# Kernel optimization log

Measured on AMD Instinct MI355X. Metric: run time of the kernel, lower is better.

The kernel has to match this reference:

```python
import jax, jax.numpy as jnp
import numpy as np

POS = np.array([[0,3,0.5],[0,3,1.5],[0,3,2.5],[0,3,3.5],[0,3,4.5],[0,3,5.5],[1,0,0],[1,6,6],[2,0,6],[2,6,0],[3,0,0],[3,6,6],[4,0,6],[4,6,0],[5,0,0],[5,6,6],[6,0,6],[6,6,0],[7,0,0],[7,6,6],[8,0,6],[8,6,0],[9,0,0],[9,6,6],[10,0,6],[10,6,0],[11,0,0],[11,6,6],[12,0,6],[12,6,0],[13,0,0],[13,6,6],[14,0,6],[14,6,0],[15,0,0],[15,6,6],[16,0,6],[16,6,0],[17,0.5,0.5],[17,3,0.5],[17,5.5,0.5],[17,0.5,3],[17,3,3],[17,5.5,3],[17,0.5,5.5],[17,3,5.5],[17,5.5,5.5]], dtype=np.float32)  # (47,3) fixed buffer

B, S, D, H, FF, HID = 512, 47, 32, 4, 2048, 256

def _ln(x, w, b, eps=1e-5):
    mu = jnp.mean(x, -1, keepdims=True)
    var = jnp.mean((x - mu) ** 2, -1, keepdims=True)
    return (x - mu) * jax.lax.rsqrt(var + eps) * w + b

def _encoder_layer(h, wi, bi, wo, bo, l1w, l1b, f1w, f1b, f2w, f2b, l2w, l2b):
    # torch post-norm TransformerEncoderLayer; batch_first=False => attention over axis 0
    L, N, E = h.shape
    Dh = E // H
    qkv = h @ wi.T + bi                                  # (L,N,3E)
    q, k, v = jnp.split(qkv, 3, axis=-1)
    q = q.reshape(L, N, H, Dh); k = k.reshape(L, N, H, Dh); v = v.reshape(L, N, H, Dh)
    scores = jnp.einsum('lnhd,mnhd->nhlm', q, k) * (1.0 / np.sqrt(Dh))  # (N,H,L,L)
    a = jax.nn.softmax(scores, axis=-1)
    o = jnp.einsum('nhlm,mnhd->lnhd', a, v).reshape(L, N, E)
    h = _ln(h + (o @ wo.T + bo), l1w, l1b)
    ff = jax.nn.relu(h @ f1w.T + f1b) @ f2w.T + f2b
    return _ln(h + ff, l2w, l2b)

def setup_inputs():
    key = jax.random.key(0)
    ks = list(jax.random.split(key, 24))
    rn = lambda k, s, sc=0.05: jax.random.normal(k, s, jnp.float32) * sc
    return dict(
        x=jax.random.normal(ks[0], (B, S), jnp.float32),
        w_in=rn(ks[1], (D, 1)), b_in=rn(ks[2], (D,)),
        w_pos=rn(ks[3], (D, 3)), b_pos=rn(ks[4], (D,)),
        cls_token=rn(ks[5], (1, 1, D), 1.0),
        attn_in_w=rn(ks[6], (2, 3 * D, D)), attn_in_b=rn(ks[7], (2, 3 * D)),
        attn_out_w=rn(ks[8], (2, D, D)), attn_out_b=rn(ks[9], (2, D)),
        ln1_w=jnp.ones((2, D)), ln1_b=jnp.zeros((2, D)),
        ff1_w=rn(ks[10], (2, FF, D)), ff1_b=rn(ks[11], (2, FF)),
        ff2_w=rn(ks[12], (2, D, FF)), ff2_b=rn(ks[13], (2, D)),
        ln2_w=jnp.ones((2, D)), ln2_b=jnp.zeros((2, D)),
        out_w=rn(ks[14], (1, D)), out_b=rn(ks[15], (1,)),
        mlp_w0=rn(ks[16], (HID, S)), mlp_b0=rn(ks[17], (HID,)),
        mlp_w1=rn(ks[18], (HID, HID)), mlp_b1=rn(ks[19], (HID,)),
        mlp_w2=rn(ks[20], (1, HID)), mlp_b2=rn(ks[21], (1,)),
    )

def reference(x, w_in, b_in, w_pos, b_pos, cls_token, attn_in_w, attn_in_b, attn_out_w, attn_out_b, ln1_w, ln1_b, ff1_w, ff1_b, ff2_w, ff2_b, ln2_w, ln2_b, out_w, out_b, mlp_w0, mlp_b0, mlp_w1, mlp_b1, mlp_w2, mlp_b2):
    Bn = x.shape[0]
    h = x[..., None] * w_in[:, 0] + b_in                 # Linear(1,D): (B,S,D)
    h = h + (jnp.asarray(POS) @ w_pos.T + b_pos)         # pos projection (S,D)
    cls = jnp.broadcast_to(cls_token, (Bn, 1, D))
    h = jnp.concatenate([cls, h], axis=1)                # (B,S+1,D)
    for i in range(2):
        h = _encoder_layer(h, attn_in_w[i], attn_in_b[i], attn_out_w[i], attn_out_b[i], ln1_w[i], ln1_b[i], ff1_w[i], ff1_b[i], ff2_w[i], ff2_b[i], ln2_w[i], ln2_b[i])
    out = jax.nn.relu(h[:, 1:, :] @ out_w.T + out_b)[..., 0]   # (B,S); dropout = eval identity
    o = jax.nn.relu(out @ mlp_w0.T + mlp_b0)
    o = jax.nn.relu(o @ mlp_w1.T + mlp_b1)
    o = jax.nn.relu(o @ mlp_w2.T + mlp_b2)               # MLP ends with ReLU per source
    return o
```

## Files before the change

### kernel.cpp

```cpp
#include <hip/hip_runtime.h>

#define NB 512
#define NS 47
#define NP 48
#define DIM 32
#define NFF 2048
#define NHID 256
#define NROWS (NB * NP)
#define FTOK 48

#define VSTR 520
#define PSTR 72

typedef _Float16 f16x8 __attribute__((ext_vector_type(8)));
typedef _Float16 f16x4 __attribute__((ext_vector_type(4)));
typedef float f32x4 __attribute__((ext_vector_type(4)));

__constant__ float POSC[NS * 3] = {
  0,3,0.5f, 0,3,1.5f, 0,3,2.5f, 0,3,3.5f, 0,3,4.5f, 0,3,5.5f,
  1,0,0, 1,6,6, 2,0,6, 2,6,0, 3,0,0, 3,6,6, 4,0,6, 4,6,0,
  5,0,0, 5,6,6, 6,0,6, 6,6,0, 7,0,0, 7,6,6, 8,0,6, 8,6,0,
  9,0,0, 9,6,6, 10,0,6, 10,6,0, 11,0,0, 11,6,6, 12,0,6, 12,6,0,
  13,0,0, 13,6,6, 14,0,6, 14,6,0, 15,0,0, 15,6,6, 16,0,6, 16,6,0,
  17,0.5f,0.5f, 17,3,0.5f, 17,5.5f,0.5f, 17,0.5f,3, 17,3,3, 17,5.5f,3,
  17,0.5f,5.5f, 17,3,5.5f, 17,5.5f,5.5f
};

__global__ __launch_bounds__(256) void prep_embed_kernel(
    const float* __restrict__ w1, const float* __restrict__ w2,
    _Float16* __restrict__ w1h, _Float16* __restrict__ w2h,
    const float* __restrict__ x, const float* __restrict__ w_in,
    const float* __restrict__ b_in, const float* __restrict__ w_pos,
    const float* __restrict__ b_pos, const float* __restrict__ cls,
    float* __restrict__ h) {
  const int bx = blockIdx.x;
  if (bx < 512) {
    int idx = bx * 256 + threadIdx.x;
    w1h[idx] = (_Float16)w1[idx];
    int l = idx >> 16, r = idx & 65535, d = r >> 11, ff = r & 2047;
    int dst = ((l * 64 + (ff >> 5)) * 32 + d) * 32 + (ff & 31);
    w2h[dst] = (_Float16)w2[idx];
    return;
  }
  int idx = (bx - 512) * 256 + threadIdx.x;
  int r = idx >> 5, d = idx & 31;
  int l = r / NP, n = r - l * NP;
  float v;
  if (n == 0) {
    v = cls[d];
  } else {
    int s = n - 1;
    v = x[l * NS + s] * w_in[d] + b_in[d]
      + POSC[s * 3 + 0] * w_pos[d * 3 + 0]
      + POSC[s * 3 + 1] * w_pos[d * 3 + 1]
      + POSC[s * 3 + 2] * w_pos[d * 3 + 2] + b_pos[d];
  }
  h[idx] = v;
}

__global__ __launch_bounds__(256) void kv_kernel(
    const float* __restrict__ h, const float* __restrict__ wi, const float* __restrict__ bi,
    _Float16* __restrict__ Kp, _Float16* __restrict__ Vt) {
  __shared__ float ws_[512];
  __shared__ float bs_[16];
  const int t = threadIdx.x;
  const int nh = blockIdx.x >> 1;
  const int n = nh >> 2, hh = nh & 3;
  const int l = ((blockIdx.x & 1) << 8) | t;
  for (int i = t; i < 512; i += 256) {
    int sub = i >> 8, rem = i & 255;
    int jj = rem >> 5, d = rem & 31;
    ws_[i] = wi[((sub + 1) * 32 + hh * 8 + jj) * 32 + d];
  }
  if (t < 16) bs_[t] = bi[((t >> 3) + 1) * 32 + hh * 8 + (t & 7)];
  __syncthreads();
  const float4* hrow = (const float4*)(h + (l * NP + n) * 32);
  float4 hv[8];
  #pragma unroll
  for (int i = 0; i < 8; ++i) hv[i] = hrow[i];
  f16x8 kh, kl_, vh;
  #pragma unroll
  for (int jj = 0; jj < 8; ++jj) {
    float k0 = bs_[jj], k1 = 0.f, k2 = 0.f, k3 = 0.f;
    float v0 = bs_[8 + jj], v1 = 0.f, v2 = 0.f, v3 = 0.f;
    #pragma unroll
    for (int d4 = 0; d4 < 8; ++d4) {
      float4 hvv = hv[d4];
      k0 += hvv.x * ws_[jj * 32 + 4 * d4 + 0];
      k1 += hvv.y * ws_[jj * 32 + 4 * d4 + 1];
      k2 += hvv.z * ws_[jj * 32 + 4 * d4 + 2];
      k3 += hvv.w * ws_[jj * 32 + 4 * d4 + 3];
      v0 += hvv.x * ws_[256 + jj * 32 + 4 * d4 + 0];
      v1 += hvv.y * ws_[256 + jj * 32 + 4 * d4 + 1];
      v2 += hvv.z * ws_[256 + jj * 32 + 4 * d4 + 2];
      v3 += hvv.w * ws_[256 + jj * 32 + 4 * d4 + 3];
    }
    float kv = (k0 + k1) + (k2 + k3);
    float vv = (v0 + v1) + (v2 + v3);
    kh[jj] = (_Float16)kv; kl_[jj] = (_Float16)(kv - (float)kh[jj]);
    vh[jj] = (_Float16)vv;
  }
  _Float16* kdst = Kp + ((size_t)nh * 512 + l) * 16;
  *(f16x8*)(kdst) = kh;
  *(f16x8*)(kdst + 8) = kl_;
  #pragma unroll
  for (int d = 0; d < 8; ++d) Vt[(size_t)nh * 4096 + d * 512 + l] = vh[d];
}

__global__ __launch_bounds__(256, 3) void attn_mfma_kernel(
    const float* __restrict__ h, const float* __restrict__ wi, const float* __restrict__ bi,
    const _Float16* __restrict__ Kp, const _Float16* __restrict__ Vt,
    float* __restrict__ o) {
  __shared__ alignas(16) _Float16 khi[512 * 8];
  __shared__ alignas(16) _Float16 klo[512 * 8];
  __shared__ alignas(16) _Float16 vts[8 * VSTR];
  __shared__ alignas(16) float hq_pls[4608];
  __shared__ alignas(16) _Float16 qf[128 * 16];
  __shared__ float wsq[256];
  __shared__ float bq[8];
  const int bx = blockIdx.x;
  const int nh = bx >> 2, qc = bx & 3;
  const int n = nh >> 2, hh = nh & 3;
  const int t = threadIdx.x;
  const int lane = t & 63, wv = t >> 6;
  const int c = lane & 15, g = lane >> 4;

  const _Float16* kg = Kp + (size_t)nh * 8192;
  for (int r = t; r < 512; r += 256) {
    const uint4* src = (const uint4*)(kg + r * 16);
    uint4 a = src[0], b = src[1];
    *(uint4*)(khi + r * 8) = a;
    *(uint4*)(klo + r * 8) = b;
  }
  {
    const _Float16* vg = Vt + (size_t)nh * 4096;
    for (int i = t; i < 512; i += 256) {
      int d = i >> 6, seg = i & 63;
      *(uint4*)(vts + d * VSTR + seg * 8) = *(const uint4*)(vg + d * 512 + seg * 8);
    }
  }
  wsq[t] = wi[(hh * 8 + (t & 7)) * 32 + (t >> 3)];
  if (t < 8) bq[t] = bi[hh * 8 + t];
  float* hq = hq_pls;

  #pragma unroll
  for (int rp = 0; rp < 2; ++rp) {
    {
      int row = t >> 2, quar = t & 3;
      const float4* src =
          (const float4*)(h + (((qc * 128 + rp * 64 + row) * NP) + n) * 32 + quar * 8);
      float4 a = src[0], b = src[1];
      __syncthreads();
      *(float4*)(hq + row * 36 + quar * 8) = a;
      *(float4*)(hq + row * 36 + quar * 8 + 4) = b;
    }
    __syncthreads();
    {
      int row = t >> 2, pr = t & 3;
      #pragma unroll
      for (int u = 0; u < 2; ++u) {
        int jj = pr * 2 + u;
        float a = bq[jj];
        #pragma unroll
        for (int d = 0; d < 32; ++d) a += hq[row * 36 + d] * wsq[d * 8 + jj];
        _Float16 qh = (_Float16)a;
        _Float16 ql = (_Float16)(a - (float)qh);
        qf[(rp * 64 + row) * 16 + jj] = qh;
        qf[(rp * 64 + row) * 16 + 8 + jj] = ql;
      }
    }
    __syncthreads();
  }

  const f16x8 hz = {(_Float16)0,(_Float16)0,(_Float16)0,(_Float16)0,
                    (_Float16)0,(_Float16)0,(_Float16)0,(_Float16)0};
  const f32x4 zf = {0.f, 0.f, 0.f, 0.f};
  _Float16* pls_ = (_Float16*)hq_pls;
  _Float16* mypA = pls_ + wv * (16 * PSTR);
  _Float16* mypB = pls_ + (4 + wv) * (16 * PSTR);
  const int q0A = qc * 128 + wv * 16;
  const int q0B = q0A + 64;

  f16x8 aqA = hz, aqB = hz;
  if (g < 3) {
    aqA = *(const f16x8*)(qf + (wv * 16 + c) * 16 + (g & 1) * 8);
    aqB = *(const f16x8*)(qf + (64 + wv * 16 + c) * 16 + (g & 1) * 8);
  }
  f32x4 accA = {0.f, 0.f, 0.f, 0.f}, accB = {0.f, 0.f, 0.f, 0.f};
  float lsA[4] = {0.f, 0.f, 0.f, 0.f}, lsB[4] = {0.f, 0.f, 0.f, 0.f};

  for (int ch = 0; ch < 8; ++ch) {
    const int kb = ch * 64;
    #pragma unroll
    for (int kt = 0; kt < 4; ++kt) {
      f16x8 bk = hz;
      if (g < 2)       bk = *(const f16x8*)(khi + (kb + kt * 16 + c) * 8);
      else if (g == 2) bk = *(const f16x8*)(klo + (kb + kt * 16 + c) * 8);
      f32x4 sA = __builtin_amdgcn_mfma_f32_16x16x32_f16(aqA, bk, zf, 0, 0, 0);
      f32x4 sB = __builtin_amdgcn_mfma_f32_16x16x32_f16(aqB, bk, zf, 0, 0, 0);
      #pragma unroll
      for (int r = 0; r < 4; ++r) {
        float pA = __expf(sA[r] * 0.35355339059327373f - 2.0f);
        float pB = __expf(sB[r] * 0.35355339059327373f - 2.0f);
        _Float16 phA = (_Float16)pA;
        _Float16 phB = (_Float16)pB;
        lsA[r] += (float)phA;
        lsB[r] += (float)phB;
        mypA[(g * 4 + r) * PSTR + kt * 16 + c] = phA;
        mypB[(g * 4 + r) * PSTR + kt * 16 + c] = phB;
      }
    }
    #pragma unroll
    for (int half = 0; half < 2; ++half) {
      f16x8 bv = hz;
      if (c < 8) bv = *(const f16x8*)(vts + c * VSTR + kb + half * 32 + g * 8);
      f16x8 apA = *(const f16x8*)(mypA + c * PSTR + half * 32 + g * 8);
      f16x8 apB = *(const f16x8*)(mypB + c * PSTR + half * 32 + g * 8);
      accA = __builtin_amdgcn_mfma_f32_16x16x32_f16(apA, bv, accA, 0, 0, 0);
      accB = __builtin_amdgcn_mfma_f32_16x16x32_f16(apB, bv, accB, 0, 0, 0);
    }
  }
  #pragma unroll
  for (int m = 1; m < 16; m <<= 1) {
    #pragma unroll
    for (int r = 0; r < 4; ++r) {
      lsA[r] += __shfl_xor(lsA[r], m, 64);
      lsB[r] += __shfl_xor(lsB[r], m, 64);
    }
  }
  if (c < 8) {
    #pragma unroll
    for (int r = 0; r < 4; ++r) {
      o[((q0A + g * 4 + r) * NP + n) * 32 + hh * 8 + c] = accA[r] / lsA[r];
      o[((q0B + g * 4 + r) * NP + n) * 32 + hh * 8 + c] = accB[r] / lsB[r];
    }
  }
}

__global__ __launch_bounds__(256) void proj_ln1_kernel(
    const float* __restrict__ o, const float* __restrict__ wo, const float* __restrict__ bo,
    const float* __restrict__ lw, const float* __restrict__ lb, float* __restrict__ h) {
  __shared__ float wos[32 * 33];
  __shared__ float pre[64 * 33];
  const int g = blockIdx.x, t = threadIdx.x;
  for (int i = t; i < 1024; i += 256) wos[(i >> 5) * 33 + (i & 31)] = wo[i];
  __syncthreads();
  const int subr = t >> 2, jq = t & 3;
  const int r = g * 64 + subr;
  const float4* orow = (const float4*)(o + r * 32);
  float4 ov[8];
  #pragma unroll
  for (int i = 0; i < 8; ++i) ov[i] = orow[i];
  const float* hres = h + r * 32 + jq * 8;
  #pragma unroll
  for (int jj = 0; jj < 8; ++jj) {
    int j = jq * 8 + jj;
    float a0 = bo[j], a1 = 0.f, a2 = 0.f, a3 = 0.f;
    #pragma unroll
    for (int d4 = 0; d4 < 8; ++d4) {
      float4 vv = ov[d4];
      a0 += vv.x * wos[j * 33 + 4 * d4 + 0];
      a1 += vv.y * wos[j * 33 + 4 * d4 + 1];
      a2 += vv.z * wos[j * 33 + 4 * d4 + 2];
      a3 += vv.w * wos[j * 33 + 4 * d4 + 3];
    }
    pre[subr * 33 + j] = (a0 + a1) + (a2 + a3) + hres[jj];
  }
  __syncthreads();
  if (t < 64) {
    float mu = 0.f;
    #pragma unroll
    for (int d = 0; d < 32; ++d) mu += pre[t * 33 + d];
    mu *= (1.f / 32.f);
    float var = 0.f;
    #pragma unroll
    for (int d = 0; d < 32; ++d) { float dv = pre[t * 33 + d] - mu; var += dv * dv; }
    float rs = rsqrtf(var * (1.f / 32.f) + 1e-5f);
    float* hrow = h + (g * 64 + t) * 32;
    #pragma unroll
    for (int d = 0; d < 32; ++d)
      hrow[d] = (pre[t * 33 + d] - mu) * rs * lw[d] + lb[d];
  }
}

__global__ __launch_bounds__(256, 2) void ff_fused_kernel(
    const float* __restrict__ h, const _Float16* __restrict__ w1h,
    const float* __restrict__ b1, const _Float16* __restrict__ w2h,
    const float* __restrict__ b2, const float* __restrict__ lw,
    const float* __restrict__ lb, const float* __restrict__ ow,
    const float* __restrict__ ob,
    const float* __restrict__ m0w, const float* __restrict__ m0b,
    const float* __restrict__ m1w, const float* __restrict__ m1b,
    const float* __restrict__ m2w, const float* __restrict__ m2b,
    float* __restrict__ out, int do_head) {
  __shared__ alignas(16) float yw[4][FTOK * 33];
  __shared__ alignas(16) float pre_s[FTOK * 33];
  __shared__ float sv1[48];
  __shared__ float hid[NHID];
  __shared__ float red[4];
  const int t = threadIdx.x;
  const int lane = t & 63;
  const int wv = t >> 6;
  const int nl = lane & 15;
  const int g = lane >> 4;
  const int g4 = g * 4;
  const int r0 = blockIdx.x * FTOK;

  f16x8 hfrag[3];
  #pragma unroll
  for (int tt = 0; tt < 3; ++tt) {
    const float4 h0 = *(const float4*)(h + (r0 + tt * 16 + nl) * 32 + g * 8);
    const float4 h1 = *(const float4*)(h + (r0 + tt * 16 + nl) * 32 + g * 8 + 4);
    hfrag[tt][0] = (_Float16)h0.x; hfrag[tt][1] = (_Float16)h0.y;
    hfrag[tt][2] = (_Float16)h0.z; hfrag[tt][3] = (_Float16)h0.w;
    hfrag[tt][4] = (_Float16)h1.x; hfrag[tt][5] = (_Float16)h1.y;
    hfrag[tt][6] = (_Float16)h1.z; hfrag[tt][7] = (_Float16)h1.w;
  }

  f32x4 acc0[3], acc1[3];
  #pragma unroll
  for (int tt = 0; tt < 3; ++tt) {
    acc0[tt] = (f32x4){0.f, 0.f, 0.f, 0.f};
    acc1[tt] = (f32x4){0.f, 0.f, 0.f, 0.f};
  }
  const f32x4 zero = {0.f, 0.f, 0.f, 0.f};

  for (int sc = 0; sc < 16; ++sc) {
    const int ffb = wv * 512 + sc * 32;
    f16x8 wf0 = *(const f16x8*)(w1h + (ffb + nl) * 32 + g * 8);
    f16x8 wf1 = *(const f16x8*)(w1h + (ffb + 16 + nl) * 32 + g * 8);
    float4 bv0 = *(const float4*)(b1 + ffb + g4);
    float4 bv1 = *(const float4*)(b1 + ffb + 16 + g4);
    const _Float16* cb = w2h + (ffb >> 5) * 1024;
    f16x4 a0lo = *(const f16x4*)(cb + nl * 32 + g4);
    f16x4 a0hi = *(const f16x4*)(cb + nl * 32 + 16 + g4);
    f16x4 a1lo = *(const f16x4*)(cb + (16 + nl) * 32 + g4);
    f16x4 a1hi = *(const f16x4*)(cb + (16 + nl) * 32 + 16 + g4);
    f16x8 A0, A1;
    #pragma unroll
    for (int j = 0; j < 4; ++j) {
      A0[j] = a0lo[j]; A0[4 + j] = a0hi[j];
      A1[j] = a1lo[j]; A1[4 + j] = a1hi[j];
    }
    #pragma unroll
    for (int tt = 0; tt < 3; ++tt) {
      f32x4 cc0 = __builtin_amdgcn_mfma_f32_16x16x32_f16(wf0, hfrag[tt], zero, 0, 0, 0);
      f32x4 cc1 = __builtin_amdgcn_mfma_f32_16x16x32_f16(wf1, hfrag[tt], zero, 0, 0, 0);
      f16x8 uB;
      uB[0] = (_Float16)fmaxf(cc0[0] + bv0.x, 0.f);
      uB[1] = (_Float16)fmaxf(cc0[1] + bv0.y, 0.f);
      uB[2] = (_Float16)fmaxf(cc0[2] + bv0.z, 0.f);
      uB[3] = (_Float16)fmaxf(cc0[3] + bv0.w, 0.f);
      uB[4] = (_Float16)fmaxf(cc1[0] + bv1.x, 0.f);
      uB[5] = (_Float16)fmaxf(cc1[1] + bv1.y, 0.f);
      uB[6] = (_Float16)fmaxf(cc1[2] + bv1.z, 0.f);
      uB[7] = (_Float16)fmaxf(cc1[3] + bv1.w, 0.f);
      acc0[tt] = __builtin_amdgcn_mfma_f32_16x16x32_f16(A0, uB, acc0[tt], 0, 0, 0);
      acc1[tt] = __builtin_amdgcn_mfma_f32_16x16x32_f16(A1, uB, acc1[tt], 0, 0, 0);
    }
  }
  #pragma unroll
  for (int tt = 0; tt < 3; ++tt) {
    #pragma unroll
    for (int r = 0; r < 4; ++r) {
      yw[wv][(tt * 16 + nl) * 33 + g4 + r]      = acc0[tt][r];
      yw[wv][(tt * 16 + nl) * 33 + 16 + g4 + r] = acc1[tt][r];
    }
  }
  __syncthreads();

  {
    int idx = t;
    #pragma unroll
    for (int u = 0; u < 6; ++u, idx += 256) {
      int tok = idx >> 5, d = idx & 31;
      int off = tok * 33 + d;
      float v = yw[0][off] + yw[1][off] + yw[2][off] + yw[3][off]
              + b2[d] + h[(r0 + tok) * 32 + d];
      pre_s[off] = v;
    }
  }
  __syncthreads();

  if (t < FTOK) {
    float mu = 0.f;
    #pragma unroll
    for (int d = 0; d < 32; ++d) mu += pre_s[t * 33 + d];
    mu *= (1.f / 32.f);
    float var = 0.f;
    #pragma unroll
    for (int d = 0; d < 32; ++d) { float dv = pre_s[t * 33 + d] - mu; var += dv * dv; }
    float rs = rsqrtf(var * (1.f / 32.f) + 1e-5f);
    const int rr = r0 + t;
    float* hrow = (float*)h + (size_t)rr * 32;
    float hn[32];
    #pragma unroll
    for (int d = 0; d < 32; ++d) {
      hn[d] = (pre_s[t * 33 + d] - mu) * rs * lw[d] + lb[d];
      hrow[d] = hn[d];
    }
    if (do_head && t > 0) {
      float a = ob[0];
      #pragma unroll
      for (int d = 0; d < 32; ++d) a += hn[d] * ow[d];
      sv1[t - 1] = fmaxf(a, 0.f);
    }
  }

  if (do_head) {
    __syncthreads();
    const int l = blockIdx.x;
    {
      float a = m0b[t];
      const float* wr = m0w + t * NS;
      #pragma unroll
      for (int s = 0; s < NS; ++s) a += sv1[s] * wr[s];
      hid[t] = fmaxf(a, 0.f);
    }
    __syncthreads();
    {
      float a = m1b[t];
      const float4* wr = (const float4*)(m1w + t * NHID);
      #pragma unroll 8
      for (int j4 = 0; j4 < 64; ++j4) {
        float4 w = wr[j4];
        a += hid[4 * j4 + 0] * w.x + hid[4 * j4 + 1] * w.y
           + hid[4 * j4 + 2] * w.z + hid[4 * j4 + 3] * w.w;
      }
      float h2 = fmaxf(a, 0.f);
      float part = h2 * m2w[t];
      #pragma unroll
      for (int off = 32; off > 0; off >>= 1) part += __shfl_down(part, off, 64);
      if ((t & 63) == 0) red[t >> 6] = part;
    }
    __syncthreads();
    if (t == 0) out[l] = fmaxf(red[0] + red[1] + red[2] + red[3] + m2b[0], 0.f);
  }
}

extern "C" void kernel_launch(void* const* d_in, const int* in_sizes, int n_in,
                              void* d_out, int out_size, void* d_ws, size_t ws_size,
                              hipStream_t stream) {
  (void)in_sizes; (void)n_in; (void)out_size; (void)ws_size;
  const float* x     = (const float*)d_in[0];
  const float* w_in  = (const float*)d_in[1];
  const float* b_in  = (const float*)d_in[2];
  const float* w_pos = (const float*)d_in[3];
  const float* b_pos = (const float*)d_in[4];
  const float* cls   = (const float*)d_in[5];
  const float* wi    = (const float*)d_in[6];
  const float* bi    = (const float*)d_in[7];
  const float* wo    = (const float*)d_in[8];
  const float* bo    = (const float*)d_in[9];
  const float* l1w   = (const float*)d_in[10];
  const float* l1b   = (const float*)d_in[11];
  const float* f1w   = (const float*)d_in[12];
  const float* f1b   = (const float*)d_in[13];
  const float* f2w   = (const float*)d_in[14];
  const float* f2b   = (const float*)d_in[15];
  const float* l2w   = (const float*)d_in[16];
  const float* l2b   = (const float*)d_in[17];
  const float* ow    = (const float*)d_in[18];
  const float* ob    = (const float*)d_in[19];
  const float* m0w   = (const float*)d_in[20];
  const float* m0b   = (const float*)d_in[21];
  const float* m1w   = (const float*)d_in[22];
  const float* m1b   = (const float*)d_in[23];
  const float* m2w   = (const float*)d_in[24];
  const float* m2b   = (const float*)d_in[25];
  float* out = (float*)d_out;

  float* ws   = (float*)d_ws;
  float* h    = ws;
  float* o    = ws + 786432;
  float* R2   = ws + 1572864;
  _Float16* Kp = (_Float16*)R2;
  _Float16* Vt = (_Float16*)(R2 + 786432);
  _Float16* w1h = (_Float16*)(ws + 2776576);
  _Float16* w2h = (_Float16*)(ws + 2842112);

  prep_embed_kernel<<<3584, 256, 0, stream>>>(f1w, f2w, w1h, w2h,
                                              x, w_in, b_in, w_pos, b_pos, cls, h);
  for (int L = 0; L < 2; ++L) {
    kv_kernel<<<384, 256, 0, stream>>>(h, wi + L * 3072, bi + L * 96, Kp, Vt);
    attn_mfma_kernel<<<768, 256, 0, stream>>>(h, wi + L * 3072, bi + L * 96, Kp, Vt, o);
    proj_ln1_kernel<<<384, 256, 0, stream>>>(o, wo + L * 1024, bo + L * 32,
                                             l1w + L * 32, l1b + L * 32, h);
    ff_fused_kernel<<<512, 256, 0, stream>>>(h, w1h + L * 65536, f1b + L * NFF,
                                             w2h + L * 65536, f2b + L * 32,
                                             l2w + L * 32, l2b + L * 32,
                                             ow, ob, m0w, m0b, m1w, m1b, m2w, m2b,
                                             out, L);
  }
}
```

Before: 150.6 us.

## Double-buffer FF weight chunks into LDS with async global_load_lds prefetch

The fused feed-forward kernel now stages each wave's W1 and W2 fp16 weight chunks in a double-buffered shared-memory area. It uses asynchronous global-to-LDS loads, prefetching chunk sc+1 while chunk sc runs through the MFMA loop. The goal is to hide global and L2 latency on the weight reads that previously went straight into registers each iteration. In exchange it adds 32KB of LDS per block, which may limit occupancy, and a block-wide barrier every iteration even though each wave only uses its own slice.

New measurement: 151.7 us. No clear change (+0.7%).

```diff
diff --git a/kernel.cpp b/kernel.cpp
--- a/kernel.cpp
+++ b/kernel.cpp
@@ -15,6 +15,11 @@
 typedef _Float16 f16x8 __attribute__((ext_vector_type(8)));
 typedef _Float16 f16x4 __attribute__((ext_vector_type(4)));
 typedef float f32x4 __attribute__((ext_vector_type(4)));
+
+#define GLL(gsrc, ldst)                                                     \
+  __builtin_amdgcn_global_load_lds(                                         \
+      (const __attribute__((address_space(1))) void*)(gsrc),                \
+      (__attribute__((address_space(3))) void*)(ldst), 16, 0, 0)
 
 __constant__ float POSC[NS * 3] = {
   0,3,0.5f, 0,3,1.5f, 0,3,2.5f, 0,3,3.5f, 0,3,4.5f, 0,3,5.5f,
@@ -293,6 +298,7 @@
     const float* __restrict__ m1w, const float* __restrict__ m1b,
     const float* __restrict__ m2w, const float* __restrict__ m2b,
     float* __restrict__ out, int do_head) {
+  __shared__ alignas(16) _Float16 wbuf[2 * 4 * 2048];
   __shared__ alignas(16) float yw[4][FTOK * 33];
   __shared__ alignas(16) float pre_s[FTOK * 33];
   __shared__ float sv1[48];
@@ -317,6 +323,17 @@
     hfrag[tt][6] = (_Float16)h1.z; hfrag[tt][7] = (_Float16)h1.w;
   }
 
+  {
+    const _Float16* g1 = w1h + (wv * 512) * 32;
+    const _Float16* g2 = w2h + (wv * 16) * 1024;
+    _Float16* d = wbuf + wv * 2048;
+    GLL(g1 + lane * 8,       d);
+    GLL(g1 + 512 + lane * 8, d + 512);
+    GLL(g2 + lane * 8,       d + 1024);
+    GLL(g2 + 512 + lane * 8, d + 1536);
+  }
+  __syncthreads();
+
   f32x4 acc0[3], acc1[3];
   #pragma unroll
   for (int tt = 0; tt < 3; ++tt) {
@@ -326,12 +343,19 @@
   const f32x4 zero = {0.f, 0.f, 0.f, 0.f};
 
   for (int sc = 0; sc < 16; ++sc) {
-    const int ffb = wv * 512 + sc * 32;
-    f16x8 wf0 = *(const f16x8*)(w1h + (ffb + nl) * 32 + g * 8);
-    f16x8 wf1 = *(const f16x8*)(w1h + (ffb + 16 + nl) * 32 + g * 8);
-    float4 bv0 = *(const float4*)(b1 + ffb + g4);
-    float4 bv1 = *(const float4*)(b1 + ffb + 16 + g4);
-    const _Float16* cb = w2h + (ffb >> 5) * 1024;
+    if (sc < 15) {
+      const _Float16* g1 = w1h + (wv * 512 + (sc + 1) * 32) * 32;
+      const _Float16* g2 = w2h + (wv * 16 + (sc + 1)) * 1024;
+      _Float16* d = wbuf + ((sc + 1) & 1) * 8192 + wv * 2048;
+      GLL(g1 + lane * 8,       d);
+      GLL(g1 + 512 + lane * 8, d + 512);
+      GLL(g2 + lane * 8,       d + 1024);
+      GLL(g2 + 512 + lane * 8, d + 1536);
+    }
+    const _Float16* s1 = wbuf + (sc & 1) * 8192 + wv * 2048;
+    f16x8 wf0 = *(const f16x8*)(s1 + nl * 32 + g * 8);
+    f16x8 wf1 = *(const f16x8*)(s1 + 512 + nl * 32 + g * 8);
+    const _Float16* cb = s1 + 1024;
     f16x4 a0lo = *(const f16x4*)(cb + nl * 32 + g4);
     f16x4 a0hi = *(const f16x4*)(cb + nl * 32 + 16 + g4);
     f16x4 a1lo = *(const f16x4*)(cb + (16 + nl) * 32 + g4);
@@ -342,6 +366,9 @@
       A0[j] = a0lo[j]; A0[4 + j] = a0hi[j];
       A1[j] = a1lo[j]; A1[4 + j] = a1hi[j];
     }
+    const int ffb = wv * 512 + sc * 32;
+    float4 bv0 = *(const float4*)(b1 + ffb + g4);
+    float4 bv1 = *(const float4*)(b1 + ffb + 16 + g4);
     #pragma unroll
     for (int tt = 0; tt < 3; ++tt) {
       f32x4 cc0 = __builtin_amdgcn_mfma_f32_16x16x32_f16(wf0, hfrag[tt], zero, 0, 0, 0);
@@ -358,7 +385,9 @@
       acc0[tt] = __builtin_amdgcn_mfma_f32_16x16x32_f16(A0, uB, acc0[tt], 0, 0, 0);
       acc1[tt] = __builtin_amdgcn_mfma_f32_16x16x32_f16(A1, uB, acc1[tt], 0, 0, 0);
     }
-  }
+    __syncthreads();
+  }
+
   #pragma unroll
   for (int tt = 0; tt < 3; ++tt) {
     #pragma unroll
```

## Merge all stages into one cooperative persistent megakernel with grid syncs

Applied to the files above, without the earlier changes.

Turns the prep, kv, attention, projection+LN and FFN kernels into device functions and runs them from a single cooperative kernel. Stages are separated by grid-wide barriers and blocks loop over virtual block indices, with a shared-memory arena reused across stages. The aim is to remove per-launch overhead and inter-kernel gaps across nine launches. In exchange, every stage is capped at the occupancy of the largest-LDS stage (at most 512 blocks), and it pays grid.sync costs. The old multi-kernel path remains as a fallback if the cooperative launch fails.

Measured after the change: 477.0 us. 217% more time.

```diff
diff --git a/kernel.cpp b/kernel.cpp
--- a/kernel.cpp
+++ b/kernel.cpp
@@ -1,4 +1,7 @@
 #include <hip/hip_runtime.h>
+#include <hip/hip_cooperative_groups.h>
+
+namespace cg = cooperative_groups;
 
 #define NB 512
 #define NS 47
@@ -6,7 +9,6 @@
 #define DIM 32
 #define NFF 2048
 #define NHID 256
-#define NROWS (NB * NP)
 #define FTOK 48
 
 #define VSTR 520
@@ -26,47 +28,47 @@
   17,0.5f,5.5f, 17,3,5.5f, 17,5.5f,5.5f
 };
 
-__global__ __launch_bounds__(256) void prep_embed_kernel(
-    const float* __restrict__ w1, const float* __restrict__ w2,
-    _Float16* __restrict__ w1h, _Float16* __restrict__ w2h,
-    const float* __restrict__ x, const float* __restrict__ w_in,
-    const float* __restrict__ b_in, const float* __restrict__ w_pos,
-    const float* __restrict__ b_pos, const float* __restrict__ cls,
-    float* __restrict__ h) {
-  const int bx = blockIdx.x;
-  if (bx < 512) {
-    int idx = bx * 256 + threadIdx.x;
-    w1h[idx] = (_Float16)w1[idx];
+struct MKArgs {
+  const float *x, *w_in, *b_in, *w_pos, *b_pos, *cls;
+  const float *wi, *bi, *wo, *bo, *l1w, *l1b, *f1w, *f1b, *f2w, *f2b, *l2w, *l2b;
+  const float *ow, *ob, *m0w, *m0b, *m1w, *m1b, *m2w, *m2b;
+  float *h, *o, *out;
+  _Float16 *Kp, *Vt, *w1h, *w2h;
+};
+
+
+__device__ __forceinline__ void prep_embed_body(const MKArgs& a, int vb, int t) {
+  if (vb < 512) {
+    int idx = vb * 256 + t;
+    a.w1h[idx] = (_Float16)a.f1w[idx];
     int l = idx >> 16, r = idx & 65535, d = r >> 11, ff = r & 2047;
     int dst = ((l * 64 + (ff >> 5)) * 32 + d) * 32 + (ff & 31);
-    w2h[dst] = (_Float16)w2[idx];
+    a.w2h[dst] = (_Float16)a.f2w[idx];
     return;
   }
-  int idx = (bx - 512) * 256 + threadIdx.x;
+  int idx = (vb - 512) * 256 + t;
   int r = idx >> 5, d = idx & 31;
   int l = r / NP, n = r - l * NP;
   float v;
   if (n == 0) {
-    v = cls[d];
+    v = a.cls[d];
   } else {
     int s = n - 1;
-    v = x[l * NS + s] * w_in[d] + b_in[d]
-      + POSC[s * 3 + 0] * w_pos[d * 3 + 0]
-      + POSC[s * 3 + 1] * w_pos[d * 3 + 1]
-      + POSC[s * 3 + 2] * w_pos[d * 3 + 2] + b_pos[d];
-  }
-  h[idx] = v;
-}
-
-__global__ __launch_bounds__(256) void kv_kernel(
-    const float* __restrict__ h, const float* __restrict__ wi, const float* __restrict__ bi,
-    _Float16* __restrict__ Kp, _Float16* __restrict__ Vt) {
-  __shared__ float ws_[512];
-  __shared__ float bs_[16];
-  const int t = threadIdx.x;
-  const int nh = blockIdx.x >> 1;
+    v = a.x[l * NS + s] * a.w_in[d] + a.b_in[d]
+      + POSC[s * 3 + 0] * a.w_pos[d * 3 + 0]
+      + POSC[s * 3 + 1] * a.w_pos[d * 3 + 1]
+      + POSC[s * 3 + 2] * a.w_pos[d * 3 + 2] + a.b_pos[d];
+  }
+  a.h[idx] = v;
+}
+
+__device__ __forceinline__ void kv_body(const MKArgs& a, const float* wi,
+                                        const float* bi, int vb, int t, char* arena) {
+  float* ws_ = (float*)arena;
+  float* bs_ = (float*)(arena + 2048);
+  const int nh = vb >> 1;
   const int n = nh >> 2, hh = nh & 3;
-  const int l = ((blockIdx.x & 1) << 8) | t;
+  const int l = ((vb & 1) << 8) | t;
   for (int i = t; i < 512; i += 256) {
     int sub = i >> 8, rem = i & 255;
     int jj = rem >> 5, d = rem & 31;
@@ -74,7 +76,7 @@
   }
   if (t < 16) bs_[t] = bi[((t >> 3) + 1) * 32 + hh * 8 + (t & 7)];
   __syncthreads();
-  const float4* hrow = (const float4*)(h + (l * NP + n) * 32);
+  const float4* hrow = (const float4*)(a.h + (l * NP + n) * 32);
   float4 hv[8];
   #pragma unroll
   for (int i = 0; i < 8; ++i) hv[i] = hrow[i];
@@ -100,40 +102,36 @@
     kh[jj] = (_Float16)kv; kl_[jj] = (_Float16)(kv - (float)kh[jj]);
     vh[jj] = (_Float16)vv;
   }
-  _Float16* kdst = Kp + ((size_t)nh * 512 + l) * 16;
+  _Float16* kdst = a.Kp + ((size_t)nh * 512 + l) * 16;
   *(f16x8*)(kdst) = kh;
   *(f16x8*)(kdst + 8) = kl_;
   #pragma unroll
-  for (int d = 0; d < 8; ++d) Vt[(size_t)nh * 4096 + d * 512 + l] = vh[d];
-}
-
-__global__ __launch_bounds__(256, 3) void attn_mfma_kernel(
-    const float* __restrict__ h, const float* __restrict__ wi, const float* __restrict__ bi,
-    const _Float16* __restrict__ Kp, const _Float16* __restrict__ Vt,
-    float* __restrict__ o) {
-  __shared__ alignas(16) _Float16 khi[512 * 8];
-  __shared__ alignas(16) _Float16 klo[512 * 8];
-  __shared__ alignas(16) _Float16 vts[8 * VSTR];
-  __shared__ alignas(16) float hq_pls[4608];
-  __shared__ alignas(16) _Float16 qf[128 * 16];
-  __shared__ float wsq[256];
-  __shared__ float bq[8];
-  const int bx = blockIdx.x;
-  const int nh = bx >> 2, qc = bx & 3;
+  for (int d = 0; d < 8; ++d) a.Vt[(size_t)nh * 4096 + d * 512 + l] = vh[d];
+}
+
+__device__ __forceinline__ void attn_body(const MKArgs& a, const float* wi,
+                                          const float* bi, int vb, int t, char* arena) {
+  _Float16* khi = (_Float16*)arena;
+  _Float16* klo = (_Float16*)(arena + 8192);
+  _Float16* vts = (_Float16*)(arena + 16384);
+  float* hq_pls = (float*)(arena + 24704);
+  _Float16* qf  = (_Float16*)(arena + 43136);
+  float* wsq    = (float*)(arena + 47232);
+  float* bq     = (float*)(arena + 48256);
+  const int nh = vb >> 2, qc = vb & 3;
   const int n = nh >> 2, hh = nh & 3;
-  const int t = threadIdx.x;
   const int lane = t & 63, wv = t >> 6;
   const int c = lane & 15, g = lane >> 4;
 
-  const _Float16* kg = Kp + (size_t)nh * 8192;
+  const _Float16* kg = a.Kp + (size_t)nh * 8192;
   for (int r = t; r < 512; r += 256) {
     const uint4* src = (const uint4*)(kg + r * 16);
-    uint4 a = src[0], b = src[1];
-    *(uint4*)(khi + r * 8) = a;
-    *(uint4*)(klo + r * 8) = b;
+    uint4 aa = src[0], bb = src[1];
+    *(uint4*)(khi + r * 8) = aa;
+    *(uint4*)(klo + r * 8) = bb;
   }
   {
-    const _Float16* vg = Vt + (size_t)nh * 4096;
+    const _Float16* vg = a.Vt + (size_t)nh * 4096;
     for (int i = t; i < 512; i += 256) {
       int d = i >> 6, seg = i & 63;
       *(uint4*)(vts + d * VSTR + seg * 8) = *(const uint4*)(vg + d * 512 + seg * 8);
@@ -148,11 +146,11 @@
     {
       int row = t >> 2, quar = t & 3;
       const float4* src =
-          (const float4*)(h + (((qc * 128 + rp * 64 + row) * NP) + n) * 32 + quar * 8);
-      float4 a = src[0], b = src[1];
+          (const float4*)(a.h + (((qc * 128 + rp * 64 + row) * NP) + n) * 32 + quar * 8);
+      float4 aa = src[0], bb = src[1];
       __syncthreads();
-      *(float4*)(hq + row * 36 + quar * 8) = a;
-      *(float4*)(hq + row * 36 + quar * 8 + 4) = b;
+      *(float4*)(hq + row * 36 + quar * 8) = aa;
+      *(float4*)(hq + row * 36 + quar * 8 + 4) = bb;
     }
     __syncthreads();
     {
@@ -160,11 +158,11 @@
       #pragma unroll
       for (int u = 0; u < 2; ++u) {
         int jj = pr * 2 + u;
-        float a = bq[jj];
+        float av = bq[jj];
         #pragma unroll
-        for (int d = 0; d < 32; ++d) a += hq[row * 36 + d] * wsq[d * 8 + jj];
-        _Float16 qh = (_Float16)a;
-        _Float16 ql = (_Float16)(a - (float)qh);
+        for (int d = 0; d < 32; ++d) av += hq[row * 36 + d] * wsq[d * 8 + jj];
+        _Float16 qh = (_Float16)av;
+        _Float16 ql = (_Float16)(av - (float)qh);
         qf[(rp * 64 + row) * 16 + jj] = qh;
         qf[(rp * 64 + row) * 16 + 8 + jj] = ql;
       }
@@ -231,27 +229,26 @@
   if (c < 8) {
     #pragma unroll
     for (int r = 0; r < 4; ++r) {
-      o[((q0A + g * 4 + r) * NP + n) * 32 + hh * 8 + c] = accA[r] / lsA[r];
-      o[((q0B + g * 4 + r) * NP + n) * 32 + hh * 8 + c] = accB[r] / lsB[r];
-    }
-  }
-}
-
-__global__ __launch_bounds__(256) void proj_ln1_kernel(
-    const float* __restrict__ o, const float* __restrict__ wo, const float* __restrict__ bo,
-    const float* __restrict__ lw, const float* __restrict__ lb, float* __restrict__ h) {
-  __shared__ float wos[32 * 33];
-  __shared__ float pre[64 * 33];
-  const int g = blockIdx.x, t = threadIdx.x;
+      a.o[((q0A + g * 4 + r) * NP + n) * 32 + hh * 8 + c] = accA[r] / lsA[r];
+      a.o[((q0B + g * 4 + r) * NP + n) * 32 + hh * 8 + c] = accB[r] / lsB[r];
+    }
+  }
+}
+
+__device__ __forceinline__ void proj_body(const MKArgs& a, const float* wo,
+                                          const float* bo, const float* lw,
+                                          const float* lb, int vb, int t, char* arena) {
+  float* wos = (float*)arena;
+  float* pre = (float*)(arena + 4224);
   for (int i = t; i < 1024; i += 256) wos[(i >> 5) * 33 + (i & 31)] = wo[i];
   __syncthreads();
   const int subr = t >> 2, jq = t & 3;
-  const int r = g * 64 + subr;
-  const float4* orow = (const float4*)(o + r * 32);
+  const int r = vb * 64 + subr;
+  const float4* orow = (const float4*)(a.o + r * 32);
   float4 ov[8];
   #pragma unroll
   for (int i = 0; i < 8; ++i) ov[i] = orow[i];
-  const float* hres = h + r * 32 + jq * 8;
+  const float* hres = a.h + r * 32 + jq * 8;
   #pragma unroll
   for (int jj = 0; jj < 8; ++jj) {
     int j = jq * 8 + jj;
@@ -276,41 +273,35 @@
     #pragma unroll
     for (int d = 0; d < 32; ++d) { float dv = pre[t * 33 + d] - mu; var += dv * dv; }
     float rs = rsqrtf(var * (1.f / 32.f) + 1e-5f);
-    float* hrow = h + (g * 64 + t) * 32;
+    float* hrow = a.h + (vb * 64 + t) * 32;
     #pragma unroll
     for (int d = 0; d < 32; ++d)
       hrow[d] = (pre[t * 33 + d] - mu) * rs * lw[d] + lb[d];
   }
 }
 
-__global__ __launch_bounds__(256, 2) void ff_fused_kernel(
-    const float* __restrict__ h, const _Float16* __restrict__ w1h,
-    const float* __restrict__ b1, const _Float16* __restrict__ w2h,
-    const float* __restrict__ b2, const float* __restrict__ lw,
-    const float* __restrict__ lb, const float* __restrict__ ow,
-    const float* __restrict__ ob,
-    const float* __restrict__ m0w, const float* __restrict__ m0b,
-    const float* __restrict__ m1w, const float* __restrict__ m1b,
-    const float* __restrict__ m2w, const float* __restrict__ m2b,
-    float* __restrict__ out, int do_head) {
-  __shared__ alignas(16) float yw[4][FTOK * 33];
-  __shared__ alignas(16) float pre_s[FTOK * 33];
-  __shared__ float sv1[48];
-  __shared__ float hid[NHID];
-  __shared__ float red[4];
-  const int t = threadIdx.x;
+__device__ __forceinline__ void ff_body(const MKArgs& a, const _Float16* w1h,
+                                        const float* b1, const _Float16* w2h,
+                                        const float* b2, const float* lw,
+                                        const float* lb, int do_head, int vb,
+                                        int t, char* arena) {
+  float* yw    = (float*)arena;
+  float* pre_s = (float*)(arena + 25344);
+  float* sv1   = (float*)(arena + 31680);
+  float* hid   = (float*)(arena + 31872);
+  float* red   = (float*)(arena + 32896);
   const int lane = t & 63;
   const int wv = t >> 6;
   const int nl = lane & 15;
   const int g = lane >> 4;
   const int g4 = g * 4;
-  const int r0 = blockIdx.x * FTOK;
+  const int r0 = vb * FTOK;
 
   f16x8 hfrag[3];
   #pragma unroll
   for (int tt = 0; tt < 3; ++tt) {
-    const float4 h0 = *(const float4*)(h + (r0 + tt * 16 + nl) * 32 + g * 8);
-    const float4 h1 = *(const float4*)(h + (r0 + tt * 16 + nl) * 32 + g * 8 + 4);
+    const float4 h0 = *(const float4*)(a.h + (r0 + tt * 16 + nl) * 32 + g * 8);
+    const float4 h1 = *(const float4*)(a.h + (r0 + tt * 16 + nl) * 32 + g * 8 + 4);
     hfrag[tt][0] = (_Float16)h0.x; hfrag[tt][1] = (_Float16)h0.y;
     hfrag[tt][2] = (_Float16)h0.z; hfrag[tt][3] = (_Float16)h0.w;
     hfrag[tt][4] = (_Float16)h1.x; hfrag[tt][5] = (_Float16)h1.y;
@@ -363,8 +354,8 @@
   for (int tt = 0; tt < 3; ++tt) {
     #pragma unroll
     for (int r = 0; r < 4; ++r) {
-      yw[wv][(tt * 16 + nl) * 33 + g4 + r]      = acc0[tt][r];
-      yw[wv][(tt * 16 + nl) * 33 + 16 + g4 + r] = acc1[tt][r];
+      yw[wv * (FTOK * 33) + (tt * 16 + nl) * 33 + g4 + r]      = acc0[tt][r];
+      yw[wv * (FTOK * 33) + (tt * 16 + nl) * 33 + 16 + g4 + r] = acc1[tt][r];
     }
   }
   __syncthreads();
@@ -375,8 +366,8 @@
     for (int u = 0; u < 6; ++u, idx += 256) {
       int tok = idx >> 5, d = idx & 31;
       int off = tok * 33 + d;
-      float v = yw[0][off] + yw[1][off] + yw[2][off] + yw[3][off]
-              + b2[d] + h[(r0 + tok) * 32 + d];
+      float v = yw[off] + yw[FTOK * 33 + off] + yw[2 * FTOK * 33 + off]
+              + yw[3 * FTOK * 33 + off] + b2[d] + a.h[(r0 + tok) * 32 + d];
       pre_s[off] = v;
     }
   }
@@ -392,7 +383,7 @@
     for (int d = 0; d < 32; ++d) { float dv = pre_s[t * 33 + d] - mu; var += dv * dv; }
     float rs = rsqrtf(var * (1.f / 32.f) + 1e-5f);
     const int rr = r0 + t;
-    float* hrow = (float*)h + (size_t)rr * 32;
+    float* hrow = a.h + (size_t)rr * 32;
     float hn[32];
     #pragma unroll
     for (int d = 0; d < 32; ++d) {
@@ -400,96 +391,163 @@
       hrow[d] = hn[d];
     }
     if (do_head && t > 0) {
-      float a = ob[0];
+      float av = a.ob[0];
       #pragma unroll
-      for (int d = 0; d < 32; ++d) a += hn[d] * ow[d];
-      sv1[t - 1] = fmaxf(a, 0.f);
+      for (int d = 0; d < 32; ++d) av += hn[d] * a.ow[d];
+      sv1[t - 1] = fmaxf(av, 0.f);
     }
   }
 
   if (do_head) {
     __syncthreads();
-    const int l = blockIdx.x;
+    const int l = vb;
     {
-      float a = m0b[t];
-      const float* wr = m0w + t * NS;
+      float av = a.m0b[t];
+      const float* wr = a.m0w + t * NS;
       #pragma unroll
-      for (int s = 0; s < NS; ++s) a += sv1[s] * wr[s];
-      hid[t] = fmaxf(a, 0.f);
+      for (int s = 0; s < NS; ++s) av += sv1[s] * wr[s];
+      hid[t] = fmaxf(av, 0.f);
     }
     __syncthreads();
     {
-      float a = m1b[t];
-      const float4* wr = (const float4*)(m1w + t * NHID);
+      float av = a.m1b[t];
+      const float4* wr = (const float4*)(a.m1w + t * NHID);
       #pragma unroll 8
       for (int j4 = 0; j4 < 64; ++j4) {
         float4 w = wr[j4];
-        a += hid[4 * j4 + 0] * w.x + hid[4 * j4 + 1] * w.y
-           + hid[4 * j4 + 2] * w.z + hid[4 * j4 + 3] * w.w;
+        av += hid[4 * j4 + 0] * w.x + hid[4 * j4 + 1] * w.y
+            + hid[4 * j4 + 2] * w.z + hid[4 * j4 + 3] * w.w;
       }
-      float h2 = fmaxf(a, 0.f);
-      float part = h2 * m2w[t];
+      float h2 = fmaxf(av, 0.f);
+      float part = h2 * a.m2w[t];
       #pragma unroll
       for (int off = 32; off > 0; off >>= 1) part += __shfl_down(part, off, 64);
       if ((t & 63) == 0) red[t >> 6] = part;
     }
     __syncthreads();
-    if (t == 0) out[l] = fmaxf(red[0] + red[1] + red[2] + red[3] + m2b[0], 0.f);
-  }
+    if (t == 0) a.out[l] = fmaxf(red[0] + red[1] + red[2] + red[3] + a.m2b[0], 0.f);
+  }
+}
+
+__global__ __launch_bounds__(256, 2) void megakernel(MKArgs a) {
+  __shared__ alignas(16) char arena[48384];
+  cg::grid_group grid = cg::this_grid();
+  const int bid = blockIdx.x;
+  const int nblk = gridDim.x;
+  const int t = threadIdx.x;
+
+  for (int vb = bid; vb < 3584; vb += nblk) prep_embed_body(a, vb, t);
+  grid.sync();
+
+  for (int L = 0; L < 2; ++L) {
+    const float* wiL = a.wi + L * 3072;
+    const float* biL = a.bi + L * 96;
+    for (int vb = bid; vb < 384; vb += nblk) {
+      kv_body(a, wiL, biL, vb, t, arena);
+      __syncthreads();
+    }
+    grid.sync();
+    for (int vb = bid; vb < 768; vb += nblk) {
+      attn_body(a, wiL, biL, vb, t, arena);
+      __syncthreads();
+    }
+    grid.sync();
+    for (int vb = bid; vb < 384; vb += nblk) {
+      proj_body(a, a.wo + L * 1024, a.bo + L * 32,
+                a.l1w + L * 32, a.l1b + L * 32, vb, t, arena);
+      __syncthreads();
+    }
+    grid.sync();
+    for (int vb = bid; vb < 512; vb += nblk) {
+      ff_body(a, a.w1h + L * 65536, a.f1b + L * NFF, a.w2h + L * 65536,
+              a.f2b + L * 32, a.l2w + L * 32, a.l2b + L * 32, L, vb, t, arena);
+      __syncthreads();
+    }
+    if (L == 0) grid.sync();
+  }
+}
+
+__global__ __launch_bounds__(256) void prep_embed_kernel(MKArgs a) {
+  prep_embed_body(a, blockIdx.x, threadIdx.x);
+}
+__global__ __launch_bounds__(256) void kv_kernel(MKArgs a, int L) {
+  __shared__ alignas(16) char arena[2112];
+  kv_body(a, a.wi + L * 3072, a.bi + L * 96, blockIdx.x, threadIdx.x, arena);
+}
+__global__ __launch_bounds__(256, 3) void attn_kernel(MKArgs a, int L) {
+  __shared__ alignas(16) char arena[48288];
+  attn_body(a, a.wi + L * 3072, a.bi + L * 96, blockIdx.x, threadIdx.x, arena);
+}
+__global__ __launch_bounds__(256) void proj_kernel(MKArgs a, int L) {
+  __shared__ alignas(16) char arena[12672];
+  proj_body(a, a.wo + L * 1024, a.bo + L * 32, a.l1w + L * 32, a.l1b + L * 32,
+            blockIdx.x, threadIdx.x, arena);
+}
+__global__ __launch_bounds__(256, 2) void ff_kernel(MKArgs a, int L) {
+  __shared__ alignas(16) char arena[32912];
+  ff_body(a, a.w1h + L * 65536, a.f1b + L * NFF, a.w2h + L * 65536,
+          a.f2b + L * 32, a.l2w + L * 32, a.l2b + L * 32, L,
+          blockIdx.x, threadIdx.x, arena);
 }
 
 extern "C" void kernel_launch(void* const* d_in, const int* in_sizes, int n_in,
                               void* d_out, int out_size, void* d_ws, size_t ws_size,
                               hipStream_t stream) {
   (void)in_sizes; (void)n_in; (void)out_size; (void)ws_size;
-  const float* x     = (const float*)d_in[0];
-  const float* w_in  = (const float*)d_in[1];
-  const float* b_in  = (const float*)d_in[2];
-  const float* w_pos = (const float*)d_in[3];
-  const float* b_pos = (const float*)d_in[4];
-  const float* cls   = (const float*)d_in[5];
-  const float* wi    = (const float*)d_in[6];
-  const float* bi    = (const float*)d_in[7];
-  const float* wo    = (const float*)d_in[8];
-  const float* bo    = (const float*)d_in[9];
-  const float* l1w   = (const float*)d_in[10];
-  const float* l1b   = (const float*)d_in[11];
-  const float* f1w   = (const float*)d_in[12];
-  const float* f1b   = (const float*)d_in[13];
-  const float* f2w   = (const float*)d_in[14];
-  const float* f2b   = (const float*)d_in[15];
-  const float* l2w   = (const float*)d_in[16];
-  const float* l2b   = (const float*)d_in[17];
-  const float* ow    = (const float*)d_in[18];
-  const float* ob    = (const float*)d_in[19];
-  const float* m0w   = (const float*)d_in[20];
-  const float* m0b   = (const float*)d_in[21];
-  const float* m1w   = (const float*)d_in[22];
-  const float* m1b   = (const float*)d_in[23];
-  const float* m2w   = (const float*)d_in[24];
-  const float* m2b   = (const float*)d_in[25];
-  float* out = (float*)d_out;
-
-  float* ws   = (float*)d_ws;
-  float* h    = ws;
-  float* o    = ws + 786432;
-  float* R2   = ws + 1572864;
-  _Float16* Kp = (_Float16*)R2;
-  _Float16* Vt = (_Float16*)(R2 + 786432);
-  _Float16* w1h = (_Float16*)(ws + 2776576);
-  _Float16* w2h = (_Float16*)(ws + 2842112);
-
-  prep_embed_kernel<<<3584, 256, 0, stream>>>(f1w, f2w, w1h, w2h,
-                                              x, w_in, b_in, w_pos, b_pos, cls, h);
-  for (int L = 0; L < 2; ++L) {
-    kv_kernel<<<384, 256, 0, stream>>>(h, wi + L * 3072, bi + L * 96, Kp, Vt);
-    attn_mfma_kernel<<<768, 256, 0, stream>>>(h, wi + L * 3072, bi + L * 96, Kp, Vt, o);
-    proj_ln1_kernel<<<384, 256, 0, stream>>>(o, wo + L * 1024, bo + L * 32,
-                                             l1w + L * 32, l1b + L * 32, h);
-    ff_fused_kernel<<<512, 256, 0, stream>>>(h, w1h + L * 65536, f1b + L * NFF,
-                                             w2h + L * 65536, f2b + L * 32,
-                                             l2w + L * 32, l2b + L * 32,
-                                             ow, ob, m0w, m0b, m1w, m1b, m2w, m2b,
-                                             out, L);
-  }
-}
+  float* ws = (float*)d_ws;
+  MKArgs a;
+  a.x     = (const float*)d_in[0];
+  a.w_in  = (const float*)d_in[1];
+  a.b_in  = (const float*)d_in[2];
+  a.w_pos = (const float*)d_in[3];
+  a.b_pos = (const float*)d_in[4];
+  a.cls   = (const float*)d_in[5];
+  a.wi    = (const float*)d_in[6];
+  a.bi    = (const float*)d_in[7];
+  a.wo    = (const float*)d_in[8];
+  a.bo    = (const float*)d_in[9];
+  a.l1w   = (const float*)d_in[10];
+  a.l1b   = (const float*)d_in[11];
+  a.f1w   = (const float*)d_in[12];
+  a.f1b   = (const float*)d_in[13];
+  a.f2w   = (const float*)d_in[14];
+  a.f2b   = (const float*)d_in[15];
+  a.l2w   = (const float*)d_in[16];
+  a.l2b   = (const float*)d_in[17];
+  a.ow    = (const float*)d_in[18];
+  a.ob    = (const float*)d_in[19];
+  a.m0w   = (const float*)d_in[20];
+  a.m0b   = (const float*)d_in[21];
+  a.m1w   = (const float*)d_in[22];
+  a.m1b   = (const float*)d_in[23];
+  a.m2w   = (const float*)d_in[24];
+  a.m2b   = (const float*)d_in[25];
+  a.out   = (float*)d_out;
+  a.h     = ws;
+  a.o     = ws + 786432;
+  a.Kp    = (_Float16*)(ws + 1572864);
+  a.Vt    = (_Float16*)(ws + 1572864 + 786432);
+  a.w1h   = (_Float16*)(ws + 2776576);
+  a.w2h   = (_Float16*)(ws + 2842112);
+
+  int occ = 0;
+  hipError_t err = hipErrorUnknown;
+  hipError_t eo = hipOccupancyMaxActiveBlocksPerMultiprocessor(
+      &occ, (const void*)megakernel, 256, 0);
+  if (eo == hipSuccess && occ > 0) {
+    int nblk = occ * 256;
+    if (nblk > 512) nblk = 512;
+    void* kp[] = {(void*)&a};
+    err = hipLaunchCooperativeKernel((const void*)megakernel, dim3(nblk),
+                                     dim3(256), kp, 0, stream);
+  }
+  if (err != hipSuccess) {
+    prep_embed_kernel<<<3584, 256, 0, stream>>>(a);
+    for (int L = 0; L < 2; ++L) {
+      kv_kernel<<<384, 256, 0, stream>>>(a, L);
+      attn_kernel<<<768, 256, 0, stream>>>(a, L);
+      proj_kernel<<<384, 256, 0, stream>>>(a, L);
+      ff_kernel<<<512, 256, 0, stream>>>(a, L);
+    }
+  }
+}
```
